# Kernel tuning notes

Hardware: AMD Instinct MI355X
Metric: run time of the kernel (lower is better)

## Reference

```python
import jax, jax.numpy as jnp
import numpy as np

N_BANKS = 16
BAND = 4
D = 32          # n_neurons_per_hidd_bank
N_IN = 3072     # n_input_neurons
N_OUT = 1000    # n_output_neurons
B = 8192        # batch size
IDX_INPUT = [0, 1]
IDX_OUTPUT = [14, 15]
# edge list (source, target), target-major, ascending sources per target --
# matches the torch loop order (np.where over bank_conn[:, i_target])
EDGES = [(s, t) for t in range(N_BANKS) for s in range(max(0, t - BAND), t)]
E = len(EDGES)  # 54
TGT_EDGES = [[e for e, (s, t) in enumerate(EDGES) if t == tt] for tt in range(N_BANKS)]
BN_EPS = 1e-5


def _bn(a):
    # BatchNorm1d in training mode: batch mean, biased batch variance
    m = a.mean(axis=0)
    v = a.var(axis=0)
    return (a - m) * jax.lax.rsqrt(v + BN_EPS)


def setup_inputs() -> dict:
    key = jax.random.key(0)
    ks = jax.random.split(key, 8)
    return {
        "x": jax.random.normal(ks[0], (B, N_IN), jnp.float32),
        "bn_gamma": jnp.ones((N_IN,), jnp.float32),
        "bn_beta": jnp.zeros((N_IN,), jnp.float32),
        "W_in": jax.random.normal(ks[1], (len(IDX_INPUT), N_IN, D), jnp.float32) / np.float32(np.sqrt(N_IN)),
        "b_in": jax.random.normal(ks[2], (len(IDX_INPUT), D), jnp.float32) / np.float32(np.sqrt(N_IN)),
        "Wg": jax.random.normal(ks[3], (E, D), jnp.float32) / np.float32(np.sqrt(D)),
        "Wd": jax.random.normal(ks[4], (E, D, D), jnp.float32) / np.float32(np.sqrt(D)),
        "bd": jax.random.normal(ks[5], (E, D), jnp.float32) / np.float32(np.sqrt(D)),
        "Wout": jax.random.normal(ks[6], (len(IDX_OUTPUT), D, N_OUT), jnp.float32) / np.float32(np.sqrt(D)),
    }


def reference(x, bn_gamma, bn_beta, W_in, b_in, Wg, Wd, bd, Wout):
    # input batch norm (affine)
    x = _bn(x) * bn_gamma + bn_beta
    acts = [None] * N_BANKS
    for k, i in enumerate(IDX_INPUT):
        acts[i] = jax.nn.relu(x @ W_in[k] + b_in[k])  # [B, D]
    total_gate = jnp.zeros((x.shape[0], 1), x.dtype)
    for t in range(N_BANKS):
        acc = acts[t]  # non-None only for input banks
        for e in TGT_EDGES[t]:
            s = EDGES[e][0]
            gate = jnp.clip(acts[s] @ Wg[e], 0.0, 1.0)[:, None]  # hardtanh(.,0,1), [B,1]
            total_gate = total_gate + gate
            data = acts[s] @ Wd[e] + bd[e]                       # [B, D]
            acc = gate * data if acc is None else acc + gate * data
        acts[t] = _bn(jax.nn.relu(acc))  # hidden batch norm, affine=False
    output = None
    for k, i in enumerate(IDX_OUTPUT):
        d = acts[i] @ Wout[k]  # Linear(D, N_OUT, bias=False)
        output = d if output is None else output + d
    return output, total_gate
```

## Files before the change

kernel.cpp:

```cpp
#include <hip/hip_runtime.h>


#define BATCH 8192
#define NIN 3072
#define DD 32
#define NB 16
#define NOUT 1000
#define TGOFF (BATCH * NOUT)
#define BNEPS 1e-5f
#define NBLK 512
#define ROWS 16

#define O_SUM 0
#define O_FLAG 0
#define O_SUM2 3072
#define O_STATS2 6144
#define O_TG 22528
#define ZERO_FLOATS 30720
#define O_SCALE 30720
#define O_SHIFT 33792
#define O_BIAS 36864
#define O_BP 36928
#define O_ACTS 233536
#define O_ACC (O_ACTS + 2 * BATCH * DD)

__global__ void __launch_bounds__(256) k_stats(const float* __restrict__ x, float* __restrict__ ws) {
    int c = blockIdx.x * 256 + threadIdx.x;
    const float* p = x + (size_t)blockIdx.y * 128 * NIN + c;
    float s = 0.f, s2 = 0.f;
#pragma unroll 8
    for (int i = 0; i < 128; i++) { float v = p[(size_t)i * NIN]; s += v; s2 += v * v; }
    atomicAdd(&ws[O_SUM + c], s);
    atomicAdd(&ws[O_SUM2 + c], s2);
}

__global__ void __launch_bounds__(256) k_prep(float* __restrict__ ws, const float* __restrict__ g,
                                              const float* __restrict__ b, const float* __restrict__ b_in) {
    int c = blockIdx.x * 256 + threadIdx.x;
    float mean = ws[O_SUM + c] * (1.f / BATCH);
    float var = ws[O_SUM2 + c] * (1.f / BATCH) - mean * mean;
    float sc = g[c] * rsqrtf(fmaxf(var, 0.f) + BNEPS);
    ws[O_SCALE + c] = sc;
    ws[O_SHIFT + c] = b[c] - mean * sc;
    if (c < 64) ws[O_BIAS + c] = b_in[c];
}

__global__ void __launch_bounds__(256) k_bias(float* __restrict__ ws, const float* __restrict__ W_in) {
    int bank = blockIdx.x & 1, jc = blockIdx.x >> 1;
    int d = threadIdx.x & 31, js = threadIdx.x >> 5;
    int j0 = jc * 256 + js * 32;
    float a = 0.f;
    for (int j = 0; j < 32; j++)
        a += ws[O_SHIFT + j0 + j] * W_in[(size_t)bank * NIN * DD + (size_t)(j0 + j) * DD + d];
    __shared__ float red[8][32];
    red[js][d] = a;
    __syncthreads();
    if (threadIdx.x < 32) {
        float t = 0.f;
#pragma unroll
        for (int g8 = 0; g8 < 8; g8++) t += red[g8][threadIdx.x];
        atomicAdd(&ws[O_BIAS + bank * 32 + threadIdx.x], t);
    }
}

__global__ void __launch_bounds__(256) k_bfold(float* __restrict__ ws, const float* __restrict__ W_in) {
    int idx = blockIdx.x * 256 + threadIdx.x;
    int j = idx >> 6, c = idx & 63;
    ws[O_BP + idx] = ws[O_SCALE + j] * W_in[(size_t)(c >> 5) * NIN * DD + (size_t)j * DD + (c & 31)];
}

__global__ void __launch_bounds__(256) k_gemm3(const float* __restrict__ x, float* __restrict__ ws) {
    __shared__ float xL[64][20];
    __shared__ float bL[16][64];
    int tid = threadIdx.x;
    int row0 = blockIdx.x * 64;
    int k00 = blockIdx.y * 768;
    const float* bp = ws + O_BP;
    float acc[4][4] = {};
    int tx = tid & 15, rt = tid >> 4;
    int lr = tid >> 2, lq = tid & 3;
    int br = tid >> 4, bq = tid & 15;
    for (int kc = 0; kc < 48; kc++) {
        int k0 = k00 + kc * 16;
        float4 xv = *(const float4*)&x[(size_t)(row0 + lr) * NIN + k0 + lq * 4];
        float4 bv = *(const float4*)&bp[(size_t)(k0 + br) * 64 + bq * 4];
        __syncthreads();
        *(float4*)&xL[lr][lq * 4] = xv;
        *(float4*)&bL[br][bq * 4] = bv;
        __syncthreads();
#pragma unroll
        for (int kk = 0; kk < 16; kk += 4) {
            float4 b0 = *(float4*)&bL[kk][tx * 4];
            float4 b1 = *(float4*)&bL[kk + 1][tx * 4];
            float4 b2 = *(float4*)&bL[kk + 2][tx * 4];
            float4 b3 = *(float4*)&bL[kk + 3][tx * 4];
#pragma unroll
            for (int j = 0; j < 4; j++) {
                float4 xv4 = *(float4*)&xL[rt * 4 + j][kk];
                acc[j][0] += xv4.x * b0.x + xv4.y * b1.x + xv4.z * b2.x + xv4.w * b3.x;
                acc[j][1] += xv4.x * b0.y + xv4.y * b1.y + xv4.z * b2.y + xv4.w * b3.y;
                acc[j][2] += xv4.x * b0.z + xv4.y * b1.z + xv4.z * b2.z + xv4.w * b3.z;
                acc[j][3] += xv4.x * b0.w + xv4.y * b1.w + xv4.z * b2.w + xv4.w * b3.w;
            }
        }
    }
    float* dst = ws + O_ACC + (size_t)blockIdx.y * (BATCH * 64);
#pragma unroll
    for (int j = 0; j < 4; j++) {
        float4 v = make_float4(acc[j][0], acc[j][1], acc[j][2], acc[j][3]);
        *(float4*)&dst[(size_t)(row0 + rt * 4 + j) * 64 + tx * 4] = v;
    }
}

__global__ void __launch_bounds__(256) k_act(float* __restrict__ ws) {
    __shared__ float sred[16][32];
    __shared__ float qred[16][32];
    int tid = threadIdx.x;
    int i4 = (blockIdx.x * 256 + tid) * 4;
    const float* ac = ws + O_ACC;
    float4 s0 = *(const float4*)&ac[i4];
    float4 s1 = *(const float4*)&ac[524288 + i4];
    float4 s2 = *(const float4*)&ac[1048576 + i4];
    float4 s3 = *(const float4*)&ac[1572864 + i4];
    int c = i4 & 63, row = i4 >> 6;
    const float* bias = ws + O_BIAS;
    float4 v;
    v.x = fmaxf(s0.x + s1.x + s2.x + s3.x + bias[c], 0.f);
    v.y = fmaxf(s0.y + s1.y + s2.y + s3.y + bias[c + 1], 0.f);
    v.z = fmaxf(s0.z + s1.z + s2.z + s3.z + bias[c + 2], 0.f);
    v.w = fmaxf(s0.w + s1.w + s2.w + s3.w + bias[c + 3], 0.f);
    int bank = c >> 5, dd = c & 31;
    *(float4*)&ws[O_ACTS + ((size_t)bank * BATCH + row) * DD + dd] = v;
    int r16 = tid >> 4;
    if (bank == 0) {
        *(float4*)&sred[r16][dd] = v;
        *(float4*)&qred[r16][dd] = make_float4(v.x * v.x, v.y * v.y, v.z * v.z, v.w * v.w);
    }
    __syncthreads();
    if (tid < 32) {
        float sm = 0.f, sq = 0.f;
#pragma unroll
        for (int r = 0; r < 16; r++) { sm += sred[r][tid]; sq += qred[r][tid]; }
        int slot = blockIdx.x & 15;
        float* st = ws + O_STATS2 + (size_t)slot * 64;
        atomicAdd(&st[tid], sm);
        atomicAdd(&st[32 + tid], sq);
    }
}

__global__ void __launch_bounds__(256, 2) k_banks(float* __restrict__ ws,
                                                  const float* __restrict__ Wg,
                                                  const float* __restrict__ Wd,
                                                  const float* __restrict__ bd) {
    __shared__ float ring[4][ROWS][32];
    __shared__ float asrcL[4][ROWS][32];
    __shared__ float WdL[2][4][1024];
    __shared__ float mL[4][32], ivL[4][32];
    __shared__ float red[8][64];
    int tid = threadIdx.x;
    int rg = tid >> 5, d = tid & 31;
    int row0 = blockIdx.x * ROWS;
    int slot = blockIdx.x & 15;
    float* acts = ws + O_ACTS;
    float* stats = ws + O_STATS2;
    int* flag = (int*)(ws + O_FLAG);
    float tg[2] = {0.f, 0.f};
    float cur[2];
#pragma unroll
    for (int ri = 0; ri < 2; ri++) {
        int r = rg + 8 * ri;
        ring[0][r][d] = acts[(size_t)(row0 + r) * DD + d];
        cur[ri] = acts[((size_t)BATCH + row0 + r) * DD + d];
    }
    if (tid < 32) {
        const float* st = stats;
        float sm = 0.f, sq = 0.f;
#pragma unroll
        for (int sl = 0; sl < 16; sl++) { sm += st[sl * 64 + tid]; sq += st[sl * 64 + 32 + tid]; }
        float m = sm * (1.f / BATCH);
        float var = sq * (1.f / BATCH) - m * m;
        mL[0][tid] = m;
        ivL[0][tid] = rsqrtf(fmaxf(var, 0.f) + BNEPS);
    }
    if (tid < 256) {
        ((float4*)&WdL[1][0][0])[tid] = ((const float4*)Wd)[tid];
    }
    for (int t = 1; t < 16; t++) {
        int buf = t & 1;
        int nE = t < 4 ? t : 4;
        int s0 = t - nE;
        int eb = (t <= 4) ? t * (t - 1) / 2 : 10 + 4 * (t - 5);
        if (t < 15) {
            int t2 = t + 1;
            int nE2 = t2 < 4 ? t2 : 4;
            int eb2 = (t2 <= 4) ? t2 * (t2 - 1) / 2 : 10 + 4 * (t2 - 5);
            for (int p = tid; p < nE2 * 256; p += 256)
                ((float4*)&WdL[buf ^ 1][0][0])[p] = ((const float4*)(Wd + (size_t)eb2 * 1024))[p];
        }
        float wgr[4], bdr[4];
#pragma unroll
        for (int ei = 0; ei < 4; ei++) {
            wgr[ei] = (ei < nE) ? Wg[(eb + ei) * 32 + d] : 0.f;
            bdr[ei] = (ei < nE) ? bd[(eb + ei) * 32 + d] : 0.f;
        }
        if (t > 1) {
            if (tid == 0) {
                while (__hip_atomic_load(&flag[t - 1], __ATOMIC_RELAXED, __HIP_MEMORY_SCOPE_AGENT) < NBLK)
                    __builtin_amdgcn_s_sleep(2);
            }
            __syncthreads();
            if (tid < 32) {
                const float* st = stats + (size_t)(t - 1) * 16 * 64;
                float sm = 0.f, sq = 0.f;
#pragma unroll
                for (int sl = 0; sl < 16; sl++) {
                    sm += __hip_atomic_load(&st[sl * 64 + tid], __ATOMIC_RELAXED, __HIP_MEMORY_SCOPE_AGENT);
                    sq += __hip_atomic_load(&st[sl * 64 + 32 + tid], __ATOMIC_RELAXED, __HIP_MEMORY_SCOPE_AGENT);
                }
                float m = sm * (1.f / BATCH);
                float var = sq * (1.f / BATCH) - m * m;
                mL[(t - 1) & 3][tid] = m;
                ivL[(t - 1) & 3][tid] = rsqrtf(fmaxf(var, 0.f) + BNEPS);
            }
        }
        __syncthreads();
#pragma unroll
        for (int si = 0; si < 4; si++) {
            if (si < nE) {
                int sl4 = (s0 + si) & 3;
#pragma unroll
                for (int ri = 0; ri < 2; ri++) {
                    int r = rg + 8 * ri;
                    asrcL[si][r][d] = (ring[sl4][r][d] - mL[sl4][d]) * ivL[sl4][d];
                }
            }
        }
        __syncthreads();
        float vv[2];
#pragma unroll
        for (int ri = 0; ri < 2; ri++) {
            int r = rg + 8 * ri;
            float c = (t == 1) ? cur[ri] : 0.f;
#pragma unroll
            for (int ei = 0; ei < 4; ei++) {
                if (ei < nE) {
                    float g = asrcL[ei][r][d] * wgr[ei];
                    g += __shfl_xor(g, 1); g += __shfl_xor(g, 2); g += __shfl_xor(g, 4);
                    g += __shfl_xor(g, 8); g += __shfl_xor(g, 16);
                    g = fminf(fmaxf(g, 0.f), 1.f);
                    tg[ri] += g;
                    float dat = bdr[ei];
                    const float* ar = asrcL[ei][r];
                    const float* wc = &WdL[buf][ei][d];
#pragma unroll
                    for (int k = 0; k < 32; k += 4) {
                        float4 a4 = *(const float4*)&ar[k];
                        dat += a4.x * wc[k * 32] + a4.y * wc[(k + 1) * 32]
                             + a4.z * wc[(k + 2) * 32] + a4.w * wc[(k + 3) * 32];
                    }
                    c += g * dat;
                }
            }
            vv[ri] = fmaxf(c, 0.f);
        }
        __syncthreads();
#pragma unroll
        for (int ri = 0; ri < 2; ri++) {
            int r = rg + 8 * ri;
            ring[t & 3][r][d] = vv[ri];
            if (t >= 14) acts[((size_t)t * BATCH + row0 + r) * DD + d] = vv[ri];
        }
        red[rg][d] = vv[0] + vv[1];
        red[rg][32 + d] = vv[0] * vv[0] + vv[1] * vv[1];
        __syncthreads();
        if (tid < 64) {
            float a = 0.f;
#pragma unroll
            for (int g8 = 0; g8 < 8; g8++) a += red[g8][tid];
            atomicAdd(&stats[((size_t)t * 16 + slot) * 64 + tid], a);
        }
        if (t < 15) {
            __syncthreads();
            if (tid == 0) atomicAdd(&flag[t], 1);
        }
    }
    if (d == 0) {
        ws[O_TG + row0 + rg] = tg[0];
        ws[O_TG + row0 + rg + 8] = tg[1];
    }
}

__global__ void __launch_bounds__(256) k_out(const float* __restrict__ ws, const float* __restrict__ Wout,
                                             float* __restrict__ out) {
    __shared__ float aLt[32][68];
    __shared__ float wL[32][128];
    __shared__ float mIv[2][2][32];
    int tid = threadIdx.x;
    int row0 = blockIdx.x * 64;
    int col0 = blockIdx.y * 128;
    const float* acts = ws + O_ACTS;
    if (blockIdx.y == 0 && tid < 64) out[TGOFF + row0 + tid] = ws[O_TG + row0 + tid];
    if (tid < 64) {
        int bi = tid >> 5, d = tid & 31;
        const float* st = ws + O_STATS2 + (size_t)(14 + bi) * 16 * 64;
        float sm = 0.f, sq = 0.f;
#pragma unroll
        for (int sl = 0; sl < 16; sl++) { sm += st[sl * 64 + d]; sq += st[sl * 64 + 32 + d]; }
        float m = sm * (1.f / BATCH);
        float var = sq * (1.f / BATCH) - m * m;
        mIv[bi][0][d] = m;
        mIv[bi][1][d] = rsqrtf(fmaxf(var, 0.f) + BNEPS);
    }
    int tx = tid & 31, ty = tid >> 5;
    int c4 = col0 + tx * 4;
    bool c4ok = (c4 + 3 < NOUT);
    float acc[8][4] = {};
    for (int bi = 0; bi < 2; bi++) {
        __syncthreads();
        {
            int d = tid & 31, r0 = tid >> 5;
            float m = mIv[bi][0][d], iv = mIv[bi][1][d];
            const float* ap = acts + ((size_t)(14 + bi) * BATCH + row0) * DD + d;
#pragma unroll
            for (int i = 0; i < 8; i++) {
                int r = r0 + 8 * i;
                aLt[d][r] = (ap[(size_t)r * DD] - m) * iv;
            }
        }
        {
            const float* wp = Wout + (size_t)bi * DD * NOUT + c4;
            int kk0 = tid >> 5;
#pragma unroll
            for (int i = 0; i < 4; i++) {
                int kk = kk0 + 8 * i;
                const float* wr = wp + (size_t)kk * NOUT;
                float4 v;
                if (c4ok) {
                    v = *(const float4*)wr;
                } else {
                    v.x = (c4 + 0 < NOUT) ? wr[0] : 0.f;
                    v.y = (c4 + 1 < NOUT) ? wr[1] : 0.f;
                    v.z = (c4 + 2 < NOUT) ? wr[2] : 0.f;
                    v.w = (c4 + 3 < NOUT) ? wr[3] : 0.f;
                }
                *(float4*)&wL[kk][tx * 4] = v;
            }
        }
        __syncthreads();
#pragma unroll 4
        for (int k = 0; k < 32; k++) {
            float4 w = *(float4*)&wL[k][tx * 4];
            float4 a0 = *(float4*)&aLt[k][ty * 8];
            float4 a1 = *(float4*)&aLt[k][ty * 8 + 4];
            float ar[8] = {a0.x, a0.y, a0.z, a0.w, a1.x, a1.y, a1.z, a1.w};
            float wc[4] = {w.x, w.y, w.z, w.w};
#pragma unroll
            for (int r = 0; r < 8; r++)
#pragma unroll
                for (int c = 0; c < 4; c++)
                    acc[r][c] += ar[r] * wc[c];
        }
    }
    if (c4ok) {
#pragma unroll
        for (int r = 0; r < 8; r++) {
            int row = row0 + ty * 8 + r;
            *(float4*)&out[(size_t)row * NOUT + c4] =
                make_float4(acc[r][0], acc[r][1], acc[r][2], acc[r][3]);
        }
    } else {
#pragma unroll
        for (int r = 0; r < 8; r++) {
            int row = row0 + ty * 8 + r;
#pragma unroll
            for (int c = 0; c < 4; c++)
                if (c4 + c < NOUT) out[(size_t)row * NOUT + c4 + c] = acc[r][c];
        }
    }
}

extern "C" void kernel_launch(void* const* d_in, const int* in_sizes, int n_in,
                              void* d_out, int out_size, void* d_ws, size_t ws_size,
                              hipStream_t stream) {
    (void)in_sizes; (void)n_in; (void)out_size; (void)ws_size;
    const float* x     = (const float*)d_in[0];
    const float* gamma = (const float*)d_in[1];
    const float* beta  = (const float*)d_in[2];
    const float* W_in  = (const float*)d_in[3];
    const float* b_in  = (const float*)d_in[4];
    const float* Wg    = (const float*)d_in[5];
    const float* Wd    = (const float*)d_in[6];
    const float* bd    = (const float*)d_in[7];
    const float* Wout  = (const float*)d_in[8];
    float* out = (float*)d_out;
    float* ws  = (float*)d_ws;

    hipMemsetAsync(d_ws, 0, ZERO_FLOATS * sizeof(float), stream);
    k_stats<<<dim3(12, 64), 256, 0, stream>>>(x, ws);
    k_prep<<<12, 256, 0, stream>>>(ws, gamma, beta, b_in);
    k_bias<<<24, 256, 0, stream>>>(ws, W_in);
    k_bfold<<<768, 256, 0, stream>>>(ws, W_in);
    k_gemm3<<<dim3(128, 4), 256, 0, stream>>>(x, ws);
    k_act<<<512, 256, 0, stream>>>(ws);
    hipMemsetAsync(ws + O_FLAG, 0, 16 * sizeof(int), stream);
    k_banks<<<NBLK, 256, 0, stream>>>(ws, Wg, Wd, bd);
    k_out<<<dim3(128, 8), 256, 0, stream>>>(ws, Wout, out);
}
```

Baseline: 433.0 us.

## Overlap grid barrier with older-source edge work and halve persistent block count

The persistent bank kernel now runs 256 blocks of 32 rows instead of 512 blocks of 16, and partial-stat slots drop from 16 to 4. Before waiting on the grid-wide flag for the previous bank's batch statistics, each block now computes the edges whose sources were already normalized. Only the newest-source edge is left until after the wait. Normalization is applied in place on the ring buffer once per bank, removing the separate asrcL staging pass. The aim is to hide the inter-block barrier latency behind useful work and cut per-step sync and atomic traffic, at the cost of fewer blocks, more atomic contention per slot, and a longer serialized path per block.

```diff
diff --git a/kernel.cpp b/kernel.cpp
--- a/kernel.cpp
+++ b/kernel.cpp
@@ -8,8 +8,8 @@
 #define NOUT 1000
 #define TGOFF (BATCH * NOUT)
 #define BNEPS 1e-5f
-#define NBLK 512
-#define ROWS 16
+#define NBLK 256
+#define ROWS 32
 
 #define O_SUM 0
 #define O_FLAG 0
@@ -141,7 +141,7 @@
         float sm = 0.f, sq = 0.f;
 #pragma unroll
         for (int r = 0; r < 16; r++) { sm += sred[r][tid]; sq += qred[r][tid]; }
-        int slot = blockIdx.x & 15;
+        int slot = blockIdx.x & 3;
         float* st = ws + O_STATS2 + (size_t)slot * 64;
         atomicAdd(&st[tid], sm);
         atomicAdd(&st[32 + tid], sq);
@@ -153,38 +153,43 @@
                                                   const float* __restrict__ Wd,
                                                   const float* __restrict__ bd) {
     __shared__ float ring[4][ROWS][32];
-    __shared__ float asrcL[4][ROWS][32];
     __shared__ float WdL[2][4][1024];
-    __shared__ float mL[4][32], ivL[4][32];
+    __shared__ float sred4[4][64];
+    __shared__ float m_s[32], iv_s[32];
     __shared__ float red[8][64];
     int tid = threadIdx.x;
     int rg = tid >> 5, d = tid & 31;
     int row0 = blockIdx.x * ROWS;
-    int slot = blockIdx.x & 15;
+    int slot4 = blockIdx.x & 3;
     float* acts = ws + O_ACTS;
     float* stats = ws + O_STATS2;
     int* flag = (int*)(ws + O_FLAG);
-    float tg[2] = {0.f, 0.f};
-    float cur[2];
-#pragma unroll
-    for (int ri = 0; ri < 2; ri++) {
+    float tg[4] = {0.f, 0.f, 0.f, 0.f};
+    float cur[4];
+#pragma unroll
+    for (int ri = 0; ri < 4; ri++) {
         int r = rg + 8 * ri;
         ring[0][r][d] = acts[(size_t)(row0 + r) * DD + d];
         cur[ri] = acts[((size_t)BATCH + row0 + r) * DD + d];
     }
+    sred4[tid >> 6][tid & 63] = stats[(size_t)(tid >> 6) * 64 + (tid & 63)];
+    __syncthreads();
     if (tid < 32) {
-        const float* st = stats;
-        float sm = 0.f, sq = 0.f;
-#pragma unroll
-        for (int sl = 0; sl < 16; sl++) { sm += st[sl * 64 + tid]; sq += st[sl * 64 + 32 + tid]; }
+        float sm = sred4[0][tid] + sred4[1][tid] + sred4[2][tid] + sred4[3][tid];
+        float sq = sred4[0][32 + tid] + sred4[1][32 + tid] + sred4[2][32 + tid] + sred4[3][32 + tid];
         float m = sm * (1.f / BATCH);
         float var = sq * (1.f / BATCH) - m * m;
-        mL[0][tid] = m;
-        ivL[0][tid] = rsqrtf(fmaxf(var, 0.f) + BNEPS);
-    }
-    if (tid < 256) {
-        ((float4*)&WdL[1][0][0])[tid] = ((const float4*)Wd)[tid];
-    }
+        m_s[tid] = m;
+        iv_s[tid] = rsqrtf(fmaxf(var, 0.f) + BNEPS);
+    }
+    ((float4*)&WdL[1][0][0])[tid] = ((const float4*)Wd)[tid];
+    __syncthreads();
+#pragma unroll
+    for (int ri = 0; ri < 4; ri++) {
+        int r = rg + 8 * ri;
+        ring[0][r][d] = (ring[0][r][d] - m_s[d]) * iv_s[d];
+    }
+    __syncthreads();
     for (int t = 1; t < 16; t++) {
         int buf = t & 1;
         int nE = t < 4 ? t : 4;
@@ -203,54 +208,23 @@
             wgr[ei] = (ei < nE) ? Wg[(eb + ei) * 32 + d] : 0.f;
             bdr[ei] = (ei < nE) ? bd[(eb + ei) * 32 + d] : 0.f;
         }
-        if (t > 1) {
-            if (tid == 0) {
-                while (__hip_atomic_load(&flag[t - 1], __ATOMIC_RELAXED, __HIP_MEMORY_SCOPE_AGENT) < NBLK)
-                    __builtin_amdgcn_s_sleep(2);
-            }
-            __syncthreads();
-            if (tid < 32) {
-                const float* st = stats + (size_t)(t - 1) * 16 * 64;
-                float sm = 0.f, sq = 0.f;
-#pragma unroll
-                for (int sl = 0; sl < 16; sl++) {
-                    sm += __hip_atomic_load(&st[sl * 64 + tid], __ATOMIC_RELAXED, __HIP_MEMORY_SCOPE_AGENT);
-                    sq += __hip_atomic_load(&st[sl * 64 + 32 + tid], __ATOMIC_RELAXED, __HIP_MEMORY_SCOPE_AGENT);
-                }
-                float m = sm * (1.f / BATCH);
-                float var = sq * (1.f / BATCH) - m * m;
-                mL[(t - 1) & 3][tid] = m;
-                ivL[(t - 1) & 3][tid] = rsqrtf(fmaxf(var, 0.f) + BNEPS);
-            }
-        }
-        __syncthreads();
-#pragma unroll
-        for (int si = 0; si < 4; si++) {
-            if (si < nE) {
-                int sl4 = (s0 + si) & 3;
-#pragma unroll
-                for (int ri = 0; ri < 2; ri++) {
+        float c_[4];
+#pragma unroll
+        for (int ri = 0; ri < 4; ri++) c_[ri] = (t == 1) ? cur[ri] : 0.f;
+#pragma unroll
+        for (int ei = 0; ei < 3; ei++) {
+            if (ei < nE - 1) {
+                int sl = (s0 + ei) & 3;
+#pragma unroll
+                for (int ri = 0; ri < 4; ri++) {
                     int r = rg + 8 * ri;
-                    asrcL[si][r][d] = (ring[sl4][r][d] - mL[sl4][d]) * ivL[sl4][d];
-                }
-            }
-        }
-        __syncthreads();
-        float vv[2];
-#pragma unroll
-        for (int ri = 0; ri < 2; ri++) {
-            int r = rg + 8 * ri;
-            float c = (t == 1) ? cur[ri] : 0.f;
-#pragma unroll
-            for (int ei = 0; ei < 4; ei++) {
-                if (ei < nE) {
-                    float g = asrcL[ei][r][d] * wgr[ei];
+                    float g = ring[sl][r][d] * wgr[ei];
                     g += __shfl_xor(g, 1); g += __shfl_xor(g, 2); g += __shfl_xor(g, 4);
                     g += __shfl_xor(g, 8); g += __shfl_xor(g, 16);
                     g = fminf(fmaxf(g, 0.f), 1.f);
                     tg[ri] += g;
                     float dat = bdr[ei];
-                    const float* ar = asrcL[ei][r];
+                    const float* ar = ring[sl][r];
                     const float* wc = &WdL[buf][ei][d];
 #pragma unroll
                     for (int k = 0; k < 32; k += 4) {
@@ -258,26 +232,78 @@
                         dat += a4.x * wc[k * 32] + a4.y * wc[(k + 1) * 32]
                              + a4.z * wc[(k + 2) * 32] + a4.w * wc[(k + 3) * 32];
                     }
-                    c += g * dat;
+                    c_[ri] += g * dat;
                 }
             }
-            vv[ri] = fmaxf(c, 0.f);
-        }
-        __syncthreads();
-#pragma unroll
-        for (int ri = 0; ri < 2; ri++) {
+        }
+        if (t > 1) {
+            if (tid == 0) {
+                while (__hip_atomic_load(&flag[t - 1], __ATOMIC_RELAXED, __HIP_MEMORY_SCOPE_AGENT) < NBLK)
+                    __builtin_amdgcn_s_sleep(8);
+            }
+            __syncthreads();
+            sred4[tid >> 6][tid & 63] = __hip_atomic_load(
+                &stats[((size_t)(t - 1) * 4 + (tid >> 6)) * 64 + (tid & 63)],
+                __ATOMIC_RELAXED, __HIP_MEMORY_SCOPE_AGENT);
+            __syncthreads();
+            if (tid < 32) {
+                float sm = sred4[0][tid] + sred4[1][tid] + sred4[2][tid] + sred4[3][tid];
+                float sq = sred4[0][32 + tid] + sred4[1][32 + tid] + sred4[2][32 + tid] + sred4[3][32 + tid];
+                float m = sm * (1.f / BATCH);
+                float var = sq * (1.f / BATCH) - m * m;
+                m_s[tid] = m;
+                iv_s[tid] = rsqrtf(fmaxf(var, 0.f) + BNEPS);
+            }
+            __syncthreads();
+            int sl = (t - 1) & 3;
+#pragma unroll
+            for (int ri = 0; ri < 4; ri++) {
+                int r = rg + 8 * ri;
+                ring[sl][r][d] = (ring[sl][r][d] - m_s[d]) * iv_s[d];
+            }
+            __syncthreads();
+        }
+        {
+            int ei = nE - 1;
+            int sl = (t - 1) & 3;
+#pragma unroll
+            for (int ri = 0; ri < 4; ri++) {
+                int r = rg + 8 * ri;
+                float g = ring[sl][r][d] * wgr[ei];
+                g += __shfl_xor(g, 1); g += __shfl_xor(g, 2); g += __shfl_xor(g, 4);
+                g += __shfl_xor(g, 8); g += __shfl_xor(g, 16);
+                g = fminf(fmaxf(g, 0.f), 1.f);
+                tg[ri] += g;
+                float dat = bdr[ei];
+                const float* ar = ring[sl][r];
+                const float* wc = &WdL[buf][ei][d];
+#pragma unroll
+                for (int k = 0; k < 32; k += 4) {
+                    float4 a4 = *(const float4*)&ar[k];
+                    dat += a4.x * wc[k * 32] + a4.y * wc[(k + 1) * 32]
+                         + a4.z * wc[(k + 2) * 32] + a4.w * wc[(k + 3) * 32];
+                }
+                c_[ri] += g * dat;
+            }
+        }
+        float vv[4];
+#pragma unroll
+        for (int ri = 0; ri < 4; ri++) vv[ri] = fmaxf(c_[ri], 0.f);
+        __syncthreads();
+#pragma unroll
+        for (int ri = 0; ri < 4; ri++) {
             int r = rg + 8 * ri;
             ring[t & 3][r][d] = vv[ri];
             if (t >= 14) acts[((size_t)t * BATCH + row0 + r) * DD + d] = vv[ri];
         }
-        red[rg][d] = vv[0] + vv[1];
-        red[rg][32 + d] = vv[0] * vv[0] + vv[1] * vv[1];
+        red[rg][d] = vv[0] + vv[1] + vv[2] + vv[3];
+        red[rg][32 + d] = vv[0] * vv[0] + vv[1] * vv[1] + vv[2] * vv[2] + vv[3] * vv[3];
         __syncthreads();
         if (tid < 64) {
             float a = 0.f;
 #pragma unroll
             for (int g8 = 0; g8 < 8; g8++) a += red[g8][tid];
-            atomicAdd(&stats[((size_t)t * 16 + slot) * 64 + tid], a);
+            atomicAdd(&stats[((size_t)t * 4 + slot4) * 64 + tid], a);
         }
         if (t < 15) {
             __syncthreads();
@@ -285,8 +311,8 @@
         }
     }
     if (d == 0) {
-        ws[O_TG + row0 + rg] = tg[0];
-        ws[O_TG + row0 + rg + 8] = tg[1];
+#pragma unroll
+        for (int ri = 0; ri < 4; ri++) ws[O_TG + row0 + rg + 8 * ri] = tg[ri];
     }
 }
 
@@ -302,10 +328,10 @@
     if (blockIdx.y == 0 && tid < 64) out[TGOFF + row0 + tid] = ws[O_TG + row0 + tid];
     if (tid < 64) {
         int bi = tid >> 5, d = tid & 31;
-        const float* st = ws + O_STATS2 + (size_t)(14 + bi) * 16 * 64;
+        const float* st = ws + O_STATS2 + (size_t)(14 + bi) * 4 * 64;
         float sm = 0.f, sq = 0.f;
 #pragma unroll
-        for (int sl = 0; sl < 16; sl++) { sm += st[sl * 64 + d]; sq += st[sl * 64 + 32 + d]; }
+        for (int sl = 0; sl < 4; sl++) { sm += st[sl * 64 + d]; sq += st[sl * 64 + 32 + d]; }
         float m = sm * (1.f / BATCH);
         float var = sq * (1.f / BATCH) - m * m;
         mIv[bi][0][d] = m;
```

New measurement: 375.8 us. 13.2% less time.
